# Optimization experiments

Hardware: AMD Instinct MI355X
Metric: run time of the kernel (lower is better)

The kernel has to match this reference:

```python
import jax, jax.numpy as jnp
import numpy as np

# ---- hash-grid constants (from tcnn Encoding config in __init__) ----
N_LEVELS = 16
F = 2                      # n_features_per_level
LOG2_T = 19
T = 1 << LOG2_T            # hashmap entries per level
BASE_RES = 16
PER_LEVEL_SCALE = 1.447269237440378
PRIMES = np.array([1, 2654435761, 805459861], dtype=np.uint32)
# corner offsets of the unit cube, shape [8, 3]
OFFS = np.stack(np.meshgrid([0, 1], [0, 1], [0, 1], indexing='ij'), -1).reshape(8, 3)


def hash_grid_encode(x01, table):
    """x01: [N,3] in [0,1]; table: [L, T, F]. Returns [N, L*F]."""
    offs = jnp.asarray(OFFS, dtype=jnp.int32)          # [8,3]
    primes = jnp.asarray(PRIMES)                       # [3] uint32
    feats = []
    for l in range(N_LEVELS):
        scale = BASE_RES * (PER_LEVEL_SCALE ** l) - 1.0   # tcnn grid scale
        res = int(np.ceil(scale)) + 1                      # grid resolution
        pos = x01 * scale + 0.5                            # [N,3]
        pos0 = jnp.floor(pos)
        w = pos - pos0                                     # trilinear fracs [N,3]
        pos0 = pos0.astype(jnp.int32)
        corners = jnp.clip(pos0[:, None, :] + offs[None], 0, res - 1)  # [N,8,3]
        if res ** 3 <= T:
            # dense (stride) indexing fits in the table
            idx = (corners[..., 0]
                   + res * corners[..., 1]
                   + res * res * corners[..., 2]).astype(jnp.int32)    # [N,8]
        else:
            # spatial hash with uint32 wraparound multiply + xor
            cu = corners.astype(jnp.uint32)
            idx = ((cu[..., 0] * primes[0])
                   ^ (cu[..., 1] * primes[1])
                   ^ (cu[..., 2] * primes[2])) & jnp.uint32(T - 1)
            idx = idx.astype(jnp.int32)
        # trilinear weights: prod over dims of (w if offset==1 else 1-w)
        wc = jnp.where(offs[None].astype(bool), w[:, None, :], 1.0 - w[:, None, :])
        wc = wc.prod(-1)                                   # [N,8]
        g = table[l][idx]                                  # gather -> [N,8,F]
        feats.append(jnp.einsum('nc,ncf->nf', wc, g))      # [N,F]
    return jnp.concatenate(feats, -1)                      # [N, L*F]


def mlp2(x, w1, w2):
    # 2-layer bias-free MLP with ReLU, matching MLP(num_layers=2, bias=False)
    return jnp.maximum(x @ w1, 0.0) @ w2


def setup_inputs() -> dict:
    key = jax.random.key(0)
    ks = jax.random.split(key, 6)
    N = 1048576
    points = jax.random.uniform(ks[0], (N, 3), jnp.float32, -1.0, 1.0)  # in bbox [-1,1]^3
    # tcnn hash-grid init: uniform(-1e-4, 1e-4)
    hash_table = jax.random.uniform(ks[1], (N_LEVELS, T, F), jnp.float32, -1e-4, 1e-4)
    enc_dim = N_LEVELS * F  # 32
    dw1 = jax.random.normal(ks[2], (enc_dim, 64), jnp.float32) * (1.0 / np.sqrt(enc_dim))
    dw2 = jax.random.normal(ks[3], (64, 1), jnp.float32) * (1.0 / 8.0)
    fw1 = jax.random.normal(ks[4], (enc_dim, 64), jnp.float32) * (1.0 / np.sqrt(enc_dim))
    fw2 = jax.random.normal(ks[5], (64, 3), jnp.float32) * (1.0 / 8.0)
    return {"points": points, "hash_table": hash_table,
            "dw1": dw1, "dw2": dw2, "fw1": fw1, "fw2": fw2}


def reference(points, hash_table, dw1, dw2, fw1, fw2):
    # contract_to_unisphere with bbox [[-1,-1,-1],[1,1,1]] -> [0,1]^3, clamped
    x01 = jnp.clip((points + 1.0) * 0.5, 0.0, 1.0)
    enc = hash_grid_encode(x01, hash_table)               # [N, 32]
    density = jax.nn.softplus(mlp2(enc, dw1, dw2))        # [N, 1]
    color = jax.nn.sigmoid(mlp2(enc, fw1, fw2))           # [N, 3]
    return color, density
```

## Files before the change

### kernel.cpp

```cpp
#include <hip/hip_runtime.h>
#include <hip/hip_bf16.h>
#include <cmath>

#define NLV 16
#define TBL_SIZE (1u << 19)
#define NB (1 << 18)

struct LevelConsts {
    float scale[NLV];
    int   res[NLV];
    int   dense[NLV];
};

__device__ __forceinline__ unsigned int f32_to_bf16_rne(float f) {
    unsigned int u = __float_as_uint(f);
    return (u + 0x7FFFu + ((u >> 16) & 1u)) >> 16;
}
__device__ __forceinline__ unsigned int pack_bf16(float a, float b) {
    return f32_to_bf16_rne(a) | (f32_to_bf16_rne(b) << 16);
}
__device__ __forceinline__ short f32_to_bf16_s(float f) {
    return (short)f32_to_bf16_rne(f);
}
__device__ __forceinline__ float bf16lo_to_f32(unsigned int g) {
    return __uint_as_float(g << 16);
}
__device__ __forceinline__ float bf16hi_to_f32(unsigned int g) {
    return __uint_as_float(g & 0xFFFF0000u);
}

typedef __attribute__((ext_vector_type(8))) short bf16x8;
typedef __attribute__((ext_vector_type(4))) float f32x4;
typedef __attribute__((ext_vector_type(2))) unsigned int u32x2;
typedef __attribute__((ext_vector_type(4))) unsigned int u32x4;

__global__ __launch_bounds__(256) void cvt_table(const float* __restrict__ in,
                                                 unsigned int* __restrict__ out, int npairs,
                                                 unsigned int* __restrict__ hist) {
    if (hist) {
        int h = blockIdx.x * 256 + threadIdx.x;
        if (h < NB) hist[h] = 0u;
    }
    int n2 = npairs >> 1;
    int i = blockIdx.x * 256 + threadIdx.x;
    int stride = gridDim.x * 256;
    const f32x4* in4 = (const f32x4*)in;
    u32x2* out2 = (u32x2*)out;
    for (; i < n2; i += stride) {
        f32x4 v = __builtin_nontemporal_load(&in4[i]);
        u32x2 o;
        o.x = pack_bf16(v.x, v.y);
        o.y = pack_bf16(v.z, v.w);
        __builtin_nontemporal_store(o, &out2[i]);
    }
}

__device__ __forceinline__ unsigned spread3(unsigned x) {
    x &= 0x3FFu;
    x = (x | (x << 16)) & 0x030000FFu;
    x = (x | (x << 8))  & 0x0300F00Fu;
    x = (x | (x << 4))  & 0x030C30C3u;
    x = (x | (x << 2))  & 0x09249249u;
    return x;
}
__device__ __forceinline__ unsigned bucket_key(float px, float py, float pz) {
    float x = fminf(fmaxf((px + 1.0f) * 0.5f, 0.0f), 1.0f);
    float y = fminf(fmaxf((py + 1.0f) * 0.5f, 0.0f), 1.0f);
    float z = fminf(fmaxf((pz + 1.0f) * 0.5f, 0.0f), 1.0f);
    int ix = min((int)(x * 64.0f), 63);
    int iy = min((int)(y * 64.0f), 63);
    int iz = min((int)(z * 64.0f), 63);
    return spread3((unsigned)ix) | (spread3((unsigned)iy) << 1) | (spread3((unsigned)iz) << 2);
}

__global__ __launch_bounds__(256) void bucket_hist(const float* __restrict__ pts,
                                                   unsigned* __restrict__ hist, int N) {
    int i = blockIdx.x * 256 + threadIdx.x;
    int stride = gridDim.x * 256;
    for (; i < N; i += stride) {
        float px = pts[3 * i + 0];
        float py = pts[3 * i + 1];
        float pz = pts[3 * i + 2];
        atomicAdd(&hist[bucket_key(px, py, pz)], 1u);
    }
}

__device__ __forceinline__ unsigned block_excl_scan_256(unsigned v, unsigned* wtot) {
    int t = threadIdx.x;
    int lane = t & 63, wid = t >> 6;
    unsigned x = v;
#pragma unroll
    for (int d = 1; d < 64; d <<= 1) {
        unsigned y = __shfl_up(x, d, 64);
        if (lane >= d) x += y;
    }
    unsigned wex = x - v;
    if (lane == 63) wtot[wid] = x;
    __syncthreads();
    if (t == 0) {
        unsigned r = 0;
        for (int i = 0; i < 4; i++) { unsigned tt = wtot[i]; wtot[i] = r; r += tt; }
    }
    __syncthreads();
    return wex + wtot[wid];
}

__global__ __launch_bounds__(256) void scan1(const unsigned* __restrict__ hist,
                                             unsigned* __restrict__ base,
                                             unsigned* __restrict__ bsum) {
    __shared__ unsigned wtot[4];
    int t = threadIdx.x, b = blockIdx.x;
    unsigned v = hist[b * 256 + t];
    unsigned ex = block_excl_scan_256(v, wtot);
    base[b * 256 + t] = ex;
    if (t == 255) bsum[b] = ex + v;
}

__global__ __launch_bounds__(256) void scan2(unsigned* __restrict__ bsum) {
    __shared__ unsigned wtot[4];
    int t = threadIdx.x;
    unsigned s[4];
    unsigned tot = 0;
#pragma unroll
    for (int j = 0; j < 4; j++) { s[j] = bsum[4 * t + j]; tot += s[j]; }
    unsigned ex = block_excl_scan_256(tot, wtot);
    unsigned run = ex;
#pragma unroll
    for (int j = 0; j < 4; j++) { unsigned sv = s[j]; bsum[4 * t + j] = run; run += sv; }
}

__global__ __launch_bounds__(256) void scan3(unsigned* __restrict__ base,
                                             const unsigned* __restrict__ bsum) {
    base[blockIdx.x * 256 + threadIdx.x] += bsum[blockIdx.x];
}

__global__ __launch_bounds__(256) void bucket_scatter(const float* __restrict__ pts,
                                                      unsigned* __restrict__ base,
                                                      f32x4* __restrict__ spts4, int N) {
    int i = blockIdx.x * 256 + threadIdx.x;
    int stride = gridDim.x * 256;
    for (; i < N; i += stride) {
        float px = pts[3 * i + 0];
        float py = pts[3 * i + 1];
        float pz = pts[3 * i + 2];
        unsigned k = bucket_key(px, py, pz);
        unsigned pos = atomicAdd(&base[k], 1u);
        f32x4 o;
        o.x = px; o.y = py; o.z = pz; o.w = __uint_as_float((unsigned)i);
        spts4[pos] = o;
    }
}

#define ENC_P 4
template<int PSTRIDE>
__global__ __launch_bounds__(256) void encode_lvl(
    const float* __restrict__ points,
    const unsigned int* __restrict__ tbl,
    unsigned int* __restrict__ enc,
    int N, LevelConsts C)
{
    const int level = blockIdx.y;
    const float sc    = C.scale[level];
    const int   res   = C.res[level];
    const int   dense = C.dense[level];
    const unsigned int* __restrict__ t = tbl + (size_t)level * TBL_SIZE;
    unsigned int* __restrict__ eo = enc + (size_t)level * N;

    const int base = blockIdx.x * (256 * ENC_P) + threadIdx.x;

    int   pt[ENC_P];
    int   valid[ENC_P];
    float wx[ENC_P], wy[ENC_P], wz[ENC_P];
    unsigned int i0a[ENC_P][4], i1a[ENC_P][4];

#pragma unroll
    for (int q = 0; q < ENC_P; q++) {
        pt[q] = base + q * 256;
        valid[q] = pt[q] < N;
        int p = valid[q] ? pt[q] : 0;
        float px, py, pz;
        if (PSTRIDE == 4) {
            f32x4 v = *(const f32x4*)&points[(size_t)p * 4];
            px = v.x; py = v.y; pz = v.z;
        } else {
            px = points[p * 3 + 0];
            py = points[p * 3 + 1];
            pz = points[p * 3 + 2];
        }
        float x = fminf(fmaxf((px + 1.0f) * 0.5f, 0.0f), 1.0f);
        float y = fminf(fmaxf((py + 1.0f) * 0.5f, 0.0f), 1.0f);
        float z = fminf(fmaxf((pz + 1.0f) * 0.5f, 0.0f), 1.0f);

        float fx = x * sc + 0.5f;
        float fy = y * sc + 0.5f;
        float fz = z * sc + 0.5f;
        float f0x = floorf(fx), f0y = floorf(fy), f0z = floorf(fz);
        wx[q] = fx - f0x; wy[q] = fy - f0y; wz[q] = fz - f0z;
        int ix0 = min(max((int)f0x, 0), res - 1);
        int iy0 = min(max((int)f0y, 0), res - 1);
        int iz0 = min(max((int)f0z, 0), res - 1);
        int ix1 = min(ix0 + 1, res - 1);
        int iy1 = min(iy0 + 1, res - 1);
        int iz1 = min(iz0 + 1, res - 1);

#pragma unroll
        for (int m = 0; m < 4; m++) {
            unsigned int uy = (unsigned int)((m & 1) ? iy1 : iy0);
            unsigned int uz = (unsigned int)((m & 2) ? iz1 : iz0);
            unsigned int i0, i1;
            if (dense) {
                unsigned int b = (unsigned int)res * uy + (unsigned int)(res * res) * uz;
                i0 = (unsigned int)ix0 + b;
                i1 = (unsigned int)ix1 + b;
            } else {
                unsigned int H = uy * 2654435761u ^ uz * 805459861u;
                i0 = ((unsigned int)ix0 ^ H) & (TBL_SIZE - 1u);
                i1 = ((unsigned int)ix1 ^ H) & (TBL_SIZE - 1u);
            }
            i0a[q][m] = i0;
            i1a[q][m] = i1;
        }
    }

    u32x2 pr[ENC_P][4];
#pragma unroll
    for (int q = 0; q < ENC_P; q++)
#pragma unroll
        for (int m = 0; m < 4; m++)
            pr[q][m] = *(const u32x2*)(t + (i0a[q][m] & ~1u));

    unsigned int ex[ENC_P][4];
#pragma unroll
    for (int q = 0; q < ENC_P; q++)
#pragma unroll
        for (int m = 0; m < 4; m++) {
            unsigned int i0 = i0a[q][m], i1 = i1a[q][m];
            unsigned int e = 0u;
            if (i1 != (i0 ^ 1u)) e = t[i1];
            ex[q][m] = e;
        }

#pragma unroll
    for (int q = 0; q < ENC_P; q++) {
        float e0 = 0.0f, e1 = 0.0f;
        float wxq = wx[q];
#pragma unroll
        for (int m = 0; m < 4; m++) {
            unsigned int i0 = i0a[q][m], i1 = i1a[q][m];
            u32x2 P = pr[q][m];
            unsigned int v0   = (i0 & 1u) ? P.y : P.x;
            unsigned int vpar = (i0 & 1u) ? P.x : P.y;
            unsigned int v1   = (i1 == (i0 ^ 1u)) ? vpar : ex[q][m];
            float wyz = (((m & 1) ? wy[q] : 1.0f - wy[q])) *
                        (((m & 2) ? wz[q] : 1.0f - wz[q]));
            float w0 = wyz * (1.0f - wxq);
            float w1 = wyz * wxq;
            e0 = fmaf(w0, bf16lo_to_f32(v0), e0);
            e0 = fmaf(w1, bf16lo_to_f32(v1), e0);
            e1 = fmaf(w0, bf16hi_to_f32(v0), e1);
            e1 = fmaf(w1, bf16hi_to_f32(v1), e1);
        }
        if (valid[q]) __builtin_nontemporal_store(pack_bf16(e0, e1), &eo[pt[q]]);
    }
}

__global__ __launch_bounds__(256, 4) void mlp_kernel(
    const unsigned int* __restrict__ enc,
    const float* __restrict__ dw1, const float* __restrict__ dw2,
    const float* __restrict__ fw1, const float* __restrict__ fw2,
    const unsigned int* __restrict__ perm,
    float* __restrict__ out, int N, int ntiles)
{
    __shared__ unsigned int hsh[4][16][68];
    __shared__ float sOut[4][256];

    const int tid  = threadIdx.x;
    const int wave = tid >> 6;
    const int lane = tid & 63;
    const int l15 = lane & 15;
    const int quad = lane >> 4;

    bf16x8 B1[8];
#pragma unroll
    for (int nt = 0; nt < 8; nt++) {
        int col = nt * 16 + l15;
        const float* w = (col < 64) ? (dw1 + col) : (fw1 + (col - 64));
#pragma unroll
        for (int j = 0; j < 8; j++) {
            int k = quad * 8 + j;
            B1[nt][j] = f32_to_bf16_s(w[k * 64]);
        }
    }

    bf16x8 B2[4];
#pragma unroll
    for (int s = 0; s < 4; s++) {
#pragma unroll
        for (int j = 0; j < 8; j++) {
            int k_lds = s * 32 + quad * 8 + j;
            int hu = ((k_lds & 7) << 4) | (k_lds >> 3);
            float v = 0.0f;
            if (l15 == 0)      v = (hu < 64)  ? dw2[hu] : 0.0f;
            else if (l15 < 4)  v = (hu >= 64) ? fw2[(hu - 64) * 3 + (l15 - 1)] : 0.0f;
            B2[s][j] = f32_to_bf16_s(v);
        }
    }

    for (int tile = blockIdx.x; tile < ntiles; tile += gridDim.x) {
        const int wbase = tile * 256 + wave * 64;

        unsigned int au[4][4];
#pragma unroll
        for (int sub = 0; sub < 4; sub++) {
            int ptc = min(wbase + sub * 16 + l15, N - 1);
#pragma unroll
            for (int j = 0; j < 4; j++)
                au[sub][j] = enc[(size_t)(quad * 4 + j) * N + ptc];
        }

#pragma unroll
        for (int sub = 0; sub < 4; sub++) {
            union { unsigned int u[4]; bf16x8 v; } acvt;
#pragma unroll
            for (int j = 0; j < 4; j++) acvt.u[j] = au[sub][j];

            f32x4 acc1[8];
#pragma unroll
            for (int nt = 0; nt < 8; nt++) {
                acc1[nt] = (f32x4){0.0f, 0.0f, 0.0f, 0.0f};
                acc1[nt] = __builtin_amdgcn_mfma_f32_16x16x32_bf16(acvt.v, B1[nt], acc1[nt], 0, 0, 0);
            }

#pragma unroll
            for (int r = 0; r < 4; r++) {
                u32x4 pk;
#pragma unroll
                for (int d = 0; d < 4; d++) {
                    float h0 = fmaxf(acc1[2 * d + 0][r], 0.0f);
                    float h1 = fmaxf(acc1[2 * d + 1][r], 0.0f);
                    pk[d] = pack_bf16(h0, h1);
                }
                *(u32x4*)&hsh[wave][quad * 4 + r][l15 * 4] = pk;
            }

            f32x4 p0 = (f32x4){0,0,0,0}, p1 = (f32x4){0,0,0,0};
            f32x4 p2 = (f32x4){0,0,0,0}, p3 = (f32x4){0,0,0,0};
            {
                bf16x8 a0 = *(const bf16x8*)&hsh[wave][l15][0 * 16 + quad * 4];
                bf16x8 a1 = *(const bf16x8*)&hsh[wave][l15][1 * 16 + quad * 4];
                bf16x8 a2 = *(const bf16x8*)&hsh[wave][l15][2 * 16 + quad * 4];
                bf16x8 a3 = *(const bf16x8*)&hsh[wave][l15][3 * 16 + quad * 4];
                p0 = __builtin_amdgcn_mfma_f32_16x16x32_bf16(a0, B2[0], p0, 0, 0, 0);
                p1 = __builtin_amdgcn_mfma_f32_16x16x32_bf16(a1, B2[1], p1, 0, 0, 0);
                p2 = __builtin_amdgcn_mfma_f32_16x16x32_bf16(a2, B2[2], p2, 0, 0, 0);
                p3 = __builtin_amdgcn_mfma_f32_16x16x32_bf16(a3, B2[3], p3, 0, 0, 0);
            }
            f32x4 acc2;
#pragma unroll
            for (int r = 0; r < 4; r++) acc2[r] = (p0[r] + p1[r]) + (p2[r] + p3[r]);

            if (l15 < 4) {
#pragma unroll
                for (int r = 0; r < 4; r++)
                    sOut[wave][(sub * 16 + quad * 4 + r) * 4 + l15] = acc2[r];
            }
        }

        if (perm) {
            int p = wbase + lane;
            if (p < N) {
                unsigned int o = perm[(size_t)p * 4 + 3];
                f32x4 v = *(const f32x4*)&sOut[wave][lane * 4];
                float d = v[0];
                d = (d > 20.0f) ? d : log1pf(expf(d));
                out[(size_t)3 * N + o] = d;
                float r0 = 1.0f / (1.0f + expf(-v[1]));
                float g0 = 1.0f / (1.0f + expf(-v[2]));
                float b0 = 1.0f / (1.0f + expf(-v[3]));
                out[(size_t)o * 3 + 0] = r0;
                out[(size_t)o * 3 + 1] = g0;
                out[(size_t)o * 3 + 2] = b0;
            }
        } else {
            long long cmax = ((long long)N - wbase) * 3;
#pragma unroll
            for (int round = 0; round < 3; round++) {
                int f = round * 64 + lane;
                int lp = f / 3, c = f - lp * 3;
                float v = sOut[wave][lp * 4 + 1 + c];
                v = 1.0f / (1.0f + expf(-v));
                if (f < cmax) out[(size_t)wbase * 3 + f] = v;
            }
            {
                int p = wbase + lane;
                float v = sOut[wave][lane * 4];
                v = (v > 20.0f) ? v : log1pf(expf(v));
                if (p < N) out[(size_t)3 * N + p] = v;
            }
        }
    }
}

__global__ __launch_bounds__(256) void nerf_fused(
    const float* __restrict__ points,
    const float* __restrict__ table,
    const float* __restrict__ dw1, const float* __restrict__ dw2,
    const float* __restrict__ fw1, const float* __restrict__ fw2,
    float* __restrict__ out, int N, LevelConsts C)
{
    __shared__ float sD[64 * 32];
    __shared__ float sF[64 * 32];
    __shared__ float sDw2[64];
    __shared__ float sFw2[64 * 3];

    for (int idx = threadIdx.x; idx < 2048; idx += 256) {
        int i = idx >> 6;
        int j = idx & 63;
        sD[j * 32 + i] = dw1[idx];
        sF[j * 32 + i] = fw1[idx];
    }
    if (threadIdx.x < 64)  sDw2[threadIdx.x] = dw2[threadIdx.x];
    if (threadIdx.x < 192) sFw2[threadIdx.x] = fw2[threadIdx.x];
    __syncthreads();

    int gid = blockIdx.x * 256 + threadIdx.x;
    if (gid >= N) return;

    float px = points[gid * 3 + 0];
    float py = points[gid * 3 + 1];
    float pz = points[gid * 3 + 2];
    float x = fminf(fmaxf((px + 1.0f) * 0.5f, 0.0f), 1.0f);
    float y = fminf(fmaxf((py + 1.0f) * 0.5f, 0.0f), 1.0f);
    float z = fminf(fmaxf((pz + 1.0f) * 0.5f, 0.0f), 1.0f);

    float enc[32];

#pragma unroll
    for (int l = 0; l < NLV; l++) {
        const float sc = C.scale[l];
        const int   res = C.res[l];
        const int   dense = C.dense[l];
        const float* __restrict__ tbl = table + (size_t)l * TBL_SIZE * 2;

        float fx = x * sc + 0.5f;
        float fy = y * sc + 0.5f;
        float fz = z * sc + 0.5f;
        float f0x = floorf(fx), f0y = floorf(fy), f0z = floorf(fz);
        float wx = fx - f0x, wy = fy - f0y, wz = fz - f0z;
        int ix0 = min(max((int)f0x, 0), res - 1);
        int iy0 = min(max((int)f0y, 0), res - 1);
        int iz0 = min(max((int)f0z, 0), res - 1);
        int ix1 = min(ix0 + 1, res - 1);
        int iy1 = min(iy0 + 1, res - 1);
        int iz1 = min(iz0 + 1, res - 1);

        float e0 = 0.0f, e1 = 0.0f;
#pragma unroll
        for (int c = 0; c < 8; c++) {
            int cx = (c & 4) ? ix1 : ix0;
            int cy = (c & 2) ? iy1 : iy0;
            int cz = (c & 1) ? iz1 : iz0;
            float wgt = (((c & 4) ? wx : 1.0f - wx) *
                         ((c & 2) ? wy : 1.0f - wy)) *
                         ((c & 1) ? wz : 1.0f - wz);
            unsigned int idx;
            if (dense) {
                idx = (unsigned int)(cx + res * cy + res * res * cz);
            } else {
                idx = ((unsigned int)cx * 1u
                     ^ (unsigned int)cy * 2654435761u
                     ^ (unsigned int)cz * 805459861u) & (TBL_SIZE - 1u);
            }
            const float2 g = *(const float2*)(tbl + (size_t)idx * 2);
            e0 = fmaf(wgt, g.x, e0);
            e1 = fmaf(wgt, g.y, e1);
        }
        enc[2 * l + 0] = e0;
        enc[2 * l + 1] = e1;
    }

    float dacc = 0.0f, c0 = 0.0f, c1 = 0.0f, c2 = 0.0f;
    for (int j = 0; j < 64; j++) {
        float hd = 0.0f, hf = 0.0f;
        const float* __restrict__ colD = &sD[j * 32];
        const float* __restrict__ colF = &sF[j * 32];
#pragma unroll
        for (int i = 0; i < 32; i++) {
            hd = fmaf(enc[i], colD[i], hd);
            hf = fmaf(enc[i], colF[i], hf);
        }
        hd = fmaxf(hd, 0.0f);
        hf = fmaxf(hf, 0.0f);
        dacc = fmaf(hd, sDw2[j], dacc);
        c0 = fmaf(hf, sFw2[j * 3 + 0], c0);
        c1 = fmaf(hf, sFw2[j * 3 + 1], c1);
        c2 = fmaf(hf, sFw2[j * 3 + 2], c2);
    }

    float density = (dacc > 20.0f) ? dacc : log1pf(expf(dacc));
    out[gid * 3 + 0] = 1.0f / (1.0f + expf(-c0));
    out[gid * 3 + 1] = 1.0f / (1.0f + expf(-c1));
    out[gid * 3 + 2] = 1.0f / (1.0f + expf(-c2));
    out[(size_t)3 * N + gid] = density;
}

extern "C" void kernel_launch(void* const* d_in, const int* in_sizes, int n_in,
                              void* d_out, int out_size, void* d_ws, size_t ws_size,
                              hipStream_t stream) {
    const float* points = (const float*)d_in[0];
    const float* table  = (const float*)d_in[1];
    const float* dw1    = (const float*)d_in[2];
    const float* dw2    = (const float*)d_in[3];
    const float* fw1    = (const float*)d_in[4];
    const float* fw2    = (const float*)d_in[5];
    int N = in_sizes[0] / 3;

    LevelConsts C;
    for (int l = 0; l < NLV; l++) {
        double s = 16.0 * pow(1.447269237440378, (double)l) - 1.0;
        C.scale[l] = (float)s;
        int res = (int)ceil(s) + 1;
        C.res[l] = res;
        C.dense[l] = ((long long)res * res * res <= (long long)TBL_SIZE) ? 1 : 0;
    }

    auto align256 = [](size_t x) { return (x + 255) & ~(size_t)255; };
    const size_t tbl_bytes  = align256((size_t)NLV * TBL_SIZE * 4);
    const size_t enc_bytes  = align256((size_t)N * NLV * 4);
    const size_t spts_bytes = align256((size_t)N * 4 * 4);
    const size_t hist_bytes = align256((size_t)NB * 4);
    const size_t base_bytes = align256((size_t)NB * 4);
    const size_t bsum_bytes = align256((size_t)(NB / 256) * 4);
    const size_t sort_total = tbl_bytes + enc_bytes + spts_bytes
                            + hist_bytes + base_bytes + bsum_bytes;

    if (ws_size >= sort_total) {
        char* wp = (char*)d_ws;
        unsigned int* tbl_bf16 = (unsigned int*)wp;            wp += tbl_bytes;
        unsigned int* enc_ws   = (unsigned int*)wp;            wp += enc_bytes;
        f32x4*        spts4    = (f32x4*)wp;                   wp += spts_bytes;
        unsigned int* hist     = (unsigned int*)wp;            wp += hist_bytes;
        unsigned int* base     = (unsigned int*)wp;            wp += base_bytes;
        unsigned int* bsum     = (unsigned int*)wp;            wp += bsum_bytes;

        int npairs = NLV * TBL_SIZE;
        cvt_table<<<1024, 256, 0, stream>>>(table, tbl_bf16, npairs, hist);

        int pblocks = min((N + 255) / 256, 2048);
        bucket_hist<<<pblocks, 256, 0, stream>>>(points, hist, N);
        scan1<<<NB / 256, 256, 0, stream>>>(hist, base, bsum);
        scan2<<<1, 256, 0, stream>>>(bsum);
        scan3<<<NB / 256, 256, 0, stream>>>(base, bsum);
        bucket_scatter<<<pblocks, 256, 0, stream>>>(points, base, spts4, N);

        int chunks = (N + 256 * ENC_P - 1) / (256 * ENC_P);
        encode_lvl<4><<<dim3(chunks, NLV), 256, 0, stream>>>((const float*)spts4,
                                                             tbl_bf16, enc_ws, N, C);

        int ntiles = (N + 255) / 256;
        mlp_kernel<<<1792, 256, 0, stream>>>(enc_ws, dw1, dw2, fw1, fw2,
                                             (const unsigned int*)spts4,
                                             (float*)d_out, N, ntiles);
    } else if (ws_size >= tbl_bytes + enc_bytes) {
        unsigned int* tbl_bf16 = (unsigned int*)d_ws;
        unsigned int* enc_ws   = (unsigned int*)((char*)d_ws + tbl_bytes);

        int npairs = NLV * TBL_SIZE;
        cvt_table<<<1024, 256, 0, stream>>>(table, tbl_bf16, npairs, nullptr);

        int chunks = (N + 256 * ENC_P - 1) / (256 * ENC_P);
        encode_lvl<3><<<dim3(chunks, NLV), 256, 0, stream>>>(points, tbl_bf16, enc_ws, N, C);

        int ntiles = (N + 255) / 256;
        mlp_kernel<<<1792, 256, 0, stream>>>(enc_ws, dw1, dw2, fw1, fw2, nullptr,
                                             (float*)d_out, N, ntiles);
    } else {
        int blocks = (N + 255) / 256;
        nerf_fused<<<blocks, 256, 0, stream>>>(points, table, dw1, dw2, fw1, fw2,
                                               (float*)d_out, N, C);
    }
}
```

Before: 567.7 us.

## Fuse hash-grid encoding with MLP in one kernel over spatially sorted points

Replaces the separate per-level encode kernel and MLP kernel on the sorted path with one kernel. Each block encodes 256 sorted points across all 16 levels, in groups of four, into LDS and then runs the MFMA MLP directly. This removes the global round trip of the encoded features (N*16 words written and reread) and one launch. The cost is that one block now walks all levels' tables, so there is less table locality per level than with per-level grids, and the larger LDS footprint plus register pressure caps occupancy at 3 blocks.

```diff
diff --git a/kernel.cpp b/kernel.cpp
--- a/kernel.cpp
+++ b/kernel.cpp
@@ -151,8 +151,207 @@
     }
 }
 
+__global__ __launch_bounds__(256, 3) void fused_enc_mlp(
+    const f32x4* __restrict__ spts4,
+    const unsigned int* __restrict__ tbl,
+    const float* __restrict__ dw1, const float* __restrict__ dw2,
+    const float* __restrict__ fw1, const float* __restrict__ fw2,
+    float* __restrict__ out, int N, int ntiles, LevelConsts C)
+{
+    __shared__ unsigned int encLds[NLV][258];
+    __shared__ unsigned int hsh[4][16][68];
+    __shared__ float sOut[4][256];
+
+    const int tid  = threadIdx.x;
+    const int wave = tid >> 6;
+    const int lane = tid & 63;
+    const int l15 = lane & 15;
+    const int quad = lane >> 4;
+
+    bf16x8 B1[8];
+#pragma unroll
+    for (int nt = 0; nt < 8; nt++) {
+        int col = nt * 16 + l15;
+        const float* w = (col < 64) ? (dw1 + col) : (fw1 + (col - 64));
+#pragma unroll
+        for (int j = 0; j < 8; j++) {
+            int k = quad * 8 + j;
+            B1[nt][j] = f32_to_bf16_s(w[k * 64]);
+        }
+    }
+
+    bf16x8 B2[4];
+#pragma unroll
+    for (int s = 0; s < 4; s++) {
+#pragma unroll
+        for (int j = 0; j < 8; j++) {
+            int k_lds = s * 32 + quad * 8 + j;
+            int hu = ((k_lds & 7) << 4) | (k_lds >> 3);
+            float v = 0.0f;
+            if (l15 == 0)      v = (hu < 64)  ? dw2[hu] : 0.0f;
+            else if (l15 < 4)  v = (hu >= 64) ? fw2[(hu - 64) * 3 + (l15 - 1)] : 0.0f;
+            B2[s][j] = f32_to_bf16_s(v);
+        }
+    }
+
+    for (int tile = blockIdx.x; tile < ntiles; tile += gridDim.x) {
+        const int p  = tile * 256 + tid;
+        const int pc = min(p, N - 1);
+        f32x4 pv = __builtin_nontemporal_load(&spts4[pc]);
+        const float x = fminf(fmaxf((pv.x + 1.0f) * 0.5f, 0.0f), 1.0f);
+        const float y = fminf(fmaxf((pv.y + 1.0f) * 0.5f, 0.0f), 1.0f);
+        const float z = fminf(fmaxf((pv.z + 1.0f) * 0.5f, 0.0f), 1.0f);
+
+        for (int lg = 0; lg < 4; lg++) {
+            float wxa[4], wya[4], wza[4];
+            unsigned int i0a[4][4], i1a[4][4];
+#pragma unroll
+            for (int lv = 0; lv < 4; lv++) {
+                int l = lg * 4 + lv;
+                float sc  = C.scale[l];
+                int  res  = C.res[l];
+                int  dense = C.dense[l];
+                float fx = x * sc + 0.5f;
+                float fy = y * sc + 0.5f;
+                float fz = z * sc + 0.5f;
+                float f0x = floorf(fx), f0y = floorf(fy), f0z = floorf(fz);
+                wxa[lv] = fx - f0x; wya[lv] = fy - f0y; wza[lv] = fz - f0z;
+                int ix0 = min(max((int)f0x, 0), res - 1);
+                int iy0 = min(max((int)f0y, 0), res - 1);
+                int iz0 = min(max((int)f0z, 0), res - 1);
+                int ix1 = min(ix0 + 1, res - 1);
+                int iy1 = min(iy0 + 1, res - 1);
+                int iz1 = min(iz0 + 1, res - 1);
+#pragma unroll
+                for (int m = 0; m < 4; m++) {
+                    unsigned int uy = (unsigned int)((m & 1) ? iy1 : iy0);
+                    unsigned int uz = (unsigned int)((m & 2) ? iz1 : iz0);
+                    unsigned int i0, i1;
+                    if (dense) {
+                        unsigned int b = (unsigned int)res * uy + (unsigned int)(res * res) * uz;
+                        i0 = (unsigned int)ix0 + b;
+                        i1 = (unsigned int)ix1 + b;
+                    } else {
+                        unsigned int H = uy * 2654435761u ^ uz * 805459861u;
+                        i0 = ((unsigned int)ix0 ^ H) & (TBL_SIZE - 1u);
+                        i1 = ((unsigned int)ix1 ^ H) & (TBL_SIZE - 1u);
+                    }
+                    i0a[lv][m] = i0;
+                    i1a[lv][m] = i1;
+                }
+            }
+
+            u32x2 pr[4][4];
+#pragma unroll
+            for (int lv = 0; lv < 4; lv++) {
+                const unsigned int* tl = tbl + (size_t)(lg * 4 + lv) * TBL_SIZE;
+#pragma unroll
+                for (int m = 0; m < 4; m++)
+                    pr[lv][m] = *(const u32x2*)(tl + (i0a[lv][m] & ~1u));
+            }
+            unsigned int ex[4][4];
+#pragma unroll
+            for (int lv = 0; lv < 4; lv++) {
+                const unsigned int* tl = tbl + (size_t)(lg * 4 + lv) * TBL_SIZE;
+#pragma unroll
+                for (int m = 0; m < 4; m++) {
+                    unsigned int i0 = i0a[lv][m], i1 = i1a[lv][m];
+                    unsigned int e = 0u;
+                    if (i1 != (i0 ^ 1u)) e = tl[i1];
+                    ex[lv][m] = e;
+                }
+            }
+
+#pragma unroll
+            for (int lv = 0; lv < 4; lv++) {
+                float e0 = 0.0f, e1 = 0.0f;
+                float wxq = wxa[lv];
+#pragma unroll
+                for (int m = 0; m < 4; m++) {
+                    unsigned int i0 = i0a[lv][m], i1 = i1a[lv][m];
+                    u32x2 P = pr[lv][m];
+                    unsigned int v0   = (i0 & 1u) ? P.y : P.x;
+                    unsigned int vpar = (i0 & 1u) ? P.x : P.y;
+                    unsigned int v1   = (i1 == (i0 ^ 1u)) ? vpar : ex[lv][m];
+                    float wyz = (((m & 1) ? wya[lv] : 1.0f - wya[lv])) *
+                                (((m & 2) ? wza[lv] : 1.0f - wza[lv]));
+                    float w0 = wyz * (1.0f - wxq);
+                    float w1 = wyz * wxq;
+                    e0 = fmaf(w0, bf16lo_to_f32(v0), e0);
+                    e0 = fmaf(w1, bf16lo_to_f32(v1), e0);
+                    e1 = fmaf(w0, bf16hi_to_f32(v0), e1);
+                    e1 = fmaf(w1, bf16hi_to_f32(v1), e1);
+                }
+                encLds[lg * 4 + lv][tid] = pack_bf16(e0, e1);
+            }
+        }
+
+#pragma unroll
+        for (int sub = 0; sub < 4; sub++) {
+            union { unsigned int u[4]; bf16x8 v; } acvt;
+#pragma unroll
+            for (int j = 0; j < 4; j++)
+                acvt.u[j] = encLds[quad * 4 + j][wave * 64 + sub * 16 + l15];
+
+            f32x4 acc1[8];
+#pragma unroll
+            for (int nt = 0; nt < 8; nt++) {
+                acc1[nt] = (f32x4){0.0f, 0.0f, 0.0f, 0.0f};
+                acc1[nt] = __builtin_amdgcn_mfma_f32_16x16x32_bf16(acvt.v, B1[nt], acc1[nt], 0, 0, 0);
+            }
+
+#pragma unroll
+            for (int r = 0; r < 4; r++) {
+                u32x4 pk;
+#pragma unroll
+                for (int d = 0; d < 4; d++) {
+                    float h0 = fmaxf(acc1[2 * d + 0][r], 0.0f);
+                    float h1 = fmaxf(acc1[2 * d + 1][r], 0.0f);
+                    pk[d] = pack_bf16(h0, h1);
+                }
+                *(u32x4*)&hsh[wave][quad * 4 + r][l15 * 4] = pk;
+            }
+
+            f32x4 p0 = (f32x4){0,0,0,0}, p1 = (f32x4){0,0,0,0};
+            f32x4 p2 = (f32x4){0,0,0,0}, p3 = (f32x4){0,0,0,0};
+            {
+                bf16x8 a0 = *(const bf16x8*)&hsh[wave][l15][0 * 16 + quad * 4];
+                bf16x8 a1 = *(const bf16x8*)&hsh[wave][l15][1 * 16 + quad * 4];
+                bf16x8 a2 = *(const bf16x8*)&hsh[wave][l15][2 * 16 + quad * 4];
+                bf16x8 a3 = *(const bf16x8*)&hsh[wave][l15][3 * 16 + quad * 4];
+                p0 = __builtin_amdgcn_mfma_f32_16x16x32_bf16(a0, B2[0], p0, 0, 0, 0);
+                p1 = __builtin_amdgcn_mfma_f32_16x16x32_bf16(a1, B2[1], p1, 0, 0, 0);
+                p2 = __builtin_amdgcn_mfma_f32_16x16x32_bf16(a2, B2[2], p2, 0, 0, 0);
+                p3 = __builtin_amdgcn_mfma_f32_16x16x32_bf16(a3, B2[3], p3, 0, 0, 0);
+            }
+            f32x4 acc2;
+#pragma unroll
+            for (int r = 0; r < 4; r++) acc2[r] = (p0[r] + p1[r]) + (p2[r] + p3[r]);
+
+            if (l15 < 4) {
+#pragma unroll
+                for (int r = 0; r < 4; r++)
+                    sOut[wave][(sub * 16 + quad * 4 + r) * 4 + l15] = acc2[r];
+            }
+        }
+
+        if (p < N) {
+            unsigned int o = __float_as_uint(pv.w);
+            f32x4 v = *(const f32x4*)&sOut[wave][lane * 4];
+            float d = v[0];
+            d = (d > 20.0f) ? d : log1pf(expf(d));
+            out[(size_t)3 * N + o] = d;
+            float r0 = 1.0f / (1.0f + expf(-v[1]));
+            float g0 = 1.0f / (1.0f + expf(-v[2]));
+            float b0 = 1.0f / (1.0f + expf(-v[3]));
+            out[(size_t)o * 3 + 0] = r0;
+            out[(size_t)o * 3 + 1] = g0;
+            out[(size_t)o * 3 + 2] = b0;
+        }
+    }
+}
+
 #define ENC_P 4
-template<int PSTRIDE>
 __global__ __launch_bounds__(256) void encode_lvl(
     const float* __restrict__ points,
     const unsigned int* __restrict__ tbl,
@@ -178,15 +377,9 @@
         pt[q] = base + q * 256;
         valid[q] = pt[q] < N;
         int p = valid[q] ? pt[q] : 0;
-        float px, py, pz;
-        if (PSTRIDE == 4) {
-            f32x4 v = *(const f32x4*)&points[(size_t)p * 4];
-            px = v.x; py = v.y; pz = v.z;
-        } else {
-            px = points[p * 3 + 0];
-            py = points[p * 3 + 1];
-            pz = points[p * 3 + 2];
-        }
+        float px = points[p * 3 + 0];
+        float py = points[p * 3 + 1];
+        float pz = points[p * 3 + 2];
         float x = fminf(fmaxf((px + 1.0f) * 0.5f, 0.0f), 1.0f);
         float y = fminf(fmaxf((py + 1.0f) * 0.5f, 0.0f), 1.0f);
         float z = fminf(fmaxf((pz + 1.0f) * 0.5f, 0.0f), 1.0f);
@@ -268,7 +461,6 @@
     const unsigned int* __restrict__ enc,
     const float* __restrict__ dw1, const float* __restrict__ dw2,
     const float* __restrict__ fw1, const float* __restrict__ fw2,
-    const unsigned int* __restrict__ perm,
     float* __restrict__ out, int N, int ntiles)
 {
     __shared__ unsigned int hsh[4][16][68];
@@ -366,37 +558,20 @@
             }
         }
 
-        if (perm) {
+        long long cmax = ((long long)N - wbase) * 3;
+#pragma unroll
+        for (int round = 0; round < 3; round++) {
+            int f = round * 64 + lane;
+            int lp = f / 3, c = f - lp * 3;
+            float v = sOut[wave][lp * 4 + 1 + c];
+            v = 1.0f / (1.0f + expf(-v));
+            if (f < cmax) out[(size_t)wbase * 3 + f] = v;
+        }
+        {
             int p = wbase + lane;
-            if (p < N) {
-                unsigned int o = perm[(size_t)p * 4 + 3];
-                f32x4 v = *(const f32x4*)&sOut[wave][lane * 4];
-                float d = v[0];
-                d = (d > 20.0f) ? d : log1pf(expf(d));
-                out[(size_t)3 * N + o] = d;
-                float r0 = 1.0f / (1.0f + expf(-v[1]));
-                float g0 = 1.0f / (1.0f + expf(-v[2]));
-                float b0 = 1.0f / (1.0f + expf(-v[3]));
-                out[(size_t)o * 3 + 0] = r0;
-                out[(size_t)o * 3 + 1] = g0;
-                out[(size_t)o * 3 + 2] = b0;
-            }
-        } else {
-            long long cmax = ((long long)N - wbase) * 3;
-#pragma unroll
-            for (int round = 0; round < 3; round++) {
-                int f = round * 64 + lane;
-                int lp = f / 3, c = f - lp * 3;
-                float v = sOut[wave][lp * 4 + 1 + c];
-                v = 1.0f / (1.0f + expf(-v));
-                if (f < cmax) out[(size_t)wbase * 3 + f] = v;
-            }
-            {
-                int p = wbase + lane;
-                float v = sOut[wave][lane * 4];
-                v = (v > 20.0f) ? v : log1pf(expf(v));
-                if (p < N) out[(size_t)3 * N + p] = v;
-            }
+            float v = sOut[wave][lane * 4];
+            v = (v > 20.0f) ? v : log1pf(expf(v));
+            if (p < N) out[(size_t)3 * N + p] = v;
         }
     }
 }
@@ -526,18 +701,18 @@
 
     auto align256 = [](size_t x) { return (x + 255) & ~(size_t)255; };
     const size_t tbl_bytes  = align256((size_t)NLV * TBL_SIZE * 4);
-    const size_t enc_bytes  = align256((size_t)N * NLV * 4);
     const size_t spts_bytes = align256((size_t)N * 4 * 4);
     const size_t hist_bytes = align256((size_t)NB * 4);
     const size_t base_bytes = align256((size_t)NB * 4);
     const size_t bsum_bytes = align256((size_t)(NB / 256) * 4);
-    const size_t sort_total = tbl_bytes + enc_bytes + spts_bytes
-                            + hist_bytes + base_bytes + bsum_bytes;
+    const size_t enc_bytes  = align256((size_t)N * NLV * 4);
+    const size_t sort_total = tbl_bytes + spts_bytes + hist_bytes + base_bytes + bsum_bytes;
+
+    int ntiles = (N + 255) / 256;
 
     if (ws_size >= sort_total) {
         char* wp = (char*)d_ws;
         unsigned int* tbl_bf16 = (unsigned int*)wp;            wp += tbl_bytes;
-        unsigned int* enc_ws   = (unsigned int*)wp;            wp += enc_bytes;
         f32x4*        spts4    = (f32x4*)wp;                   wp += spts_bytes;
         unsigned int* hist     = (unsigned int*)wp;            wp += hist_bytes;
         unsigned int* base     = (unsigned int*)wp;            wp += base_bytes;
@@ -553,14 +728,9 @@
         scan3<<<NB / 256, 256, 0, stream>>>(base, bsum);
         bucket_scatter<<<pblocks, 256, 0, stream>>>(points, base, spts4, N);
 
-        int chunks = (N + 256 * ENC_P - 1) / (256 * ENC_P);
-        encode_lvl<4><<<dim3(chunks, NLV), 256, 0, stream>>>((const float*)spts4,
-                                                             tbl_bf16, enc_ws, N, C);
-
-        int ntiles = (N + 255) / 256;
-        mlp_kernel<<<1792, 256, 0, stream>>>(enc_ws, dw1, dw2, fw1, fw2,
-                                             (const unsigned int*)spts4,
-                                             (float*)d_out, N, ntiles);
+        int fblocks = min(ntiles, 2048);
+        fused_enc_mlp<<<fblocks, 256, 0, stream>>>(spts4, tbl_bf16, dw1, dw2, fw1, fw2,
+                                                   (float*)d_out, N, ntiles, C);
     } else if (ws_size >= tbl_bytes + enc_bytes) {
         unsigned int* tbl_bf16 = (unsigned int*)d_ws;
         unsigned int* enc_ws   = (unsigned int*)((char*)d_ws + tbl_bytes);
@@ -569,10 +739,9 @@
         cvt_table<<<1024, 256, 0, stream>>>(table, tbl_bf16, npairs, nullptr);
 
         int chunks = (N + 256 * ENC_P - 1) / (256 * ENC_P);
-        encode_lvl<3><<<dim3(chunks, NLV), 256, 0, stream>>>(points, tbl_bf16, enc_ws, N, C);
-
-        int ntiles = (N + 255) / 256;
-        mlp_kernel<<<1792, 256, 0, stream>>>(enc_ws, dw1, dw2, fw1, fw2, nullptr,
+        encode_lvl<<<dim3(chunks, NLV), 256, 0, stream>>>(points, tbl_bf16, enc_ws, N, C);
+
+        mlp_kernel<<<1792, 256, 0, stream>>>(enc_ws, dw1, dw2, fw1, fw2,
                                              (float*)d_out, N, ntiles);
     } else {
         int blocks = (N + 255) / 256;
```

New measurement: 808.6 us. 1.42x slower.

## Replace global bucket sort with per-block local sort fused with table conversion

Applied to the files above, without the earlier changes.

Replaces the global 2^18-bucket counting sort (histogram, three-pass scan, scatter) with a per-block shared-memory counting sort over 8192-point chunks on a coarser 4096-key Morton grid. That sort runs in the same launch as the bf16 table conversion, cutting five launches and the global atomics. The encode kernel now uses a flat grid and maps block IDs so each XCD handles a pair of levels, aiming to keep each level's table slice in one XCD's L2. The trade-off is that locality becomes per-chunk rather than global, which may raise gather misses in encode.

```diff
diff --git a/kernel.cpp b/kernel.cpp
--- a/kernel.cpp
+++ b/kernel.cpp
@@ -4,7 +4,10 @@
 
 #define NLV 16
 #define TBL_SIZE (1u << 19)
-#define NB (1 << 18)
+
+#define SORT_PPB 8192
+#define SORT_THREADS 512
+#define SORT_NKEYS 4096
 
 struct LevelConsts {
     float scale[NLV];
@@ -34,13 +37,113 @@
 typedef __attribute__((ext_vector_type(2))) unsigned int u32x2;
 typedef __attribute__((ext_vector_type(4))) unsigned int u32x4;
 
+__device__ __forceinline__ unsigned spread3(unsigned x) {
+    x &= 0x3FFu;
+    x = (x | (x << 16)) & 0x030000FFu;
+    x = (x | (x << 8))  & 0x0300F00Fu;
+    x = (x | (x << 4))  & 0x030C30C3u;
+    x = (x | (x << 2))  & 0x09249249u;
+    return x;
+}
+__device__ __forceinline__ unsigned key12(float px, float py, float pz) {
+    float x = fminf(fmaxf((px + 1.0f) * 0.5f, 0.0f), 1.0f);
+    float y = fminf(fmaxf((py + 1.0f) * 0.5f, 0.0f), 1.0f);
+    float z = fminf(fmaxf((pz + 1.0f) * 0.5f, 0.0f), 1.0f);
+    int ix = min((int)(x * 16.0f), 15);
+    int iy = min((int)(y * 16.0f), 15);
+    int iz = min((int)(z * 16.0f), 15);
+    return spread3((unsigned)ix) | (spread3((unsigned)iy) << 1) | (spread3((unsigned)iz) << 2);
+}
+
+__global__ __launch_bounds__(SORT_THREADS) void cvt_and_sort(
+    const float* __restrict__ tablef32, unsigned int* __restrict__ tbl_out, int npairs,
+    const float* __restrict__ pts, f32x4* __restrict__ spts4, int N, int sortBlocks)
+{
+    __shared__ unsigned hist[SORT_NKEYS];
+    __shared__ unsigned wsum[SORT_THREADS / 64];
+
+    if ((int)blockIdx.x < sortBlocks) {
+        const int sb   = blockIdx.x;
+        const int base = sb * SORT_PPB;
+        const int cnt  = min(SORT_PPB, N - base);
+        const int tid  = threadIdx.x;
+        const int lane = tid & 63, wid = tid >> 6;
+
+        for (int i = tid; i < SORT_NKEYS; i += SORT_THREADS) hist[i] = 0u;
+        __syncthreads();
+
+        unsigned short keys[16];
+#pragma unroll
+        for (int q = 0; q < 16; q++) {
+            int idx = q * SORT_THREADS + tid;
+            unsigned k = 0xFFFFu;
+            if (idx < cnt) {
+                int p = base + idx;
+                float px = pts[3 * p + 0];
+                float py = pts[3 * p + 1];
+                float pz = pts[3 * p + 2];
+                k = key12(px, py, pz);
+                atomicAdd(&hist[k], 1u);
+            }
+            keys[q] = (unsigned short)k;
+        }
+        __syncthreads();
+
+        unsigned loc[8], s = 0;
+#pragma unroll
+        for (int j = 0; j < 8; j++) { loc[j] = hist[tid * 8 + j]; s += loc[j]; }
+        unsigned x = s;
+#pragma unroll
+        for (int d = 1; d < 64; d <<= 1) {
+            unsigned y = __shfl_up(x, d, 64);
+            if (lane >= d) x += y;
+        }
+        unsigned wex = x - s;
+        if (lane == 63) wsum[wid] = x;
+        __syncthreads();
+        if (tid == 0) {
+            unsigned r = 0;
+            for (int i = 0; i < SORT_THREADS / 64; i++) { unsigned t = wsum[i]; wsum[i] = r; r += t; }
+        }
+        __syncthreads();
+        unsigned run = wex + wsum[wid];
+#pragma unroll
+        for (int j = 0; j < 8; j++) { hist[tid * 8 + j] = run; run += loc[j]; }
+        __syncthreads();
+
+#pragma unroll
+        for (int q = 0; q < 16; q++) {
+            int idx = q * SORT_THREADS + tid;
+            if (idx < cnt) {
+                int p = base + idx;
+                float px = pts[3 * p + 0];
+                float py = pts[3 * p + 1];
+                float pz = pts[3 * p + 2];
+                unsigned pos = atomicAdd(&hist[keys[q]], 1u);
+                f32x4 o;
+                o.x = px; o.y = py; o.z = pz; o.w = __uint_as_float((unsigned)p);
+                spts4[base + pos] = o;
+            }
+        }
+    } else {
+        int b = blockIdx.x - sortBlocks;
+        int n2 = npairs >> 1;
+        int i = b * SORT_THREADS + threadIdx.x;
+        int stride = ((int)gridDim.x - sortBlocks) * SORT_THREADS;
+        const f32x4* in4 = (const f32x4*)tablef32;
+        u32x2* out2 = (u32x2*)tbl_out;
+        for (; i < n2; i += stride) {
+            f32x4 v = __builtin_nontemporal_load(&in4[i]);
+            u32x2 o;
+            o.x = pack_bf16(v.x, v.y);
+            o.y = pack_bf16(v.z, v.w);
+            __builtin_nontemporal_store(o, &out2[i]);
+        }
+    }
+}
+
 __global__ __launch_bounds__(256) void cvt_table(const float* __restrict__ in,
-                                                 unsigned int* __restrict__ out, int npairs,
-                                                 unsigned int* __restrict__ hist) {
-    if (hist) {
-        int h = blockIdx.x * 256 + threadIdx.x;
-        if (h < NB) hist[h] = 0u;
-    }
+                                                 unsigned int* __restrict__ out, int npairs) {
     int n2 = npairs >> 1;
     int i = blockIdx.x * 256 + threadIdx.x;
     int stride = gridDim.x * 256;
@@ -55,102 +158,6 @@
     }
 }
 
-__device__ __forceinline__ unsigned spread3(unsigned x) {
-    x &= 0x3FFu;
-    x = (x | (x << 16)) & 0x030000FFu;
-    x = (x | (x << 8))  & 0x0300F00Fu;
-    x = (x | (x << 4))  & 0x030C30C3u;
-    x = (x | (x << 2))  & 0x09249249u;
-    return x;
-}
-__device__ __forceinline__ unsigned bucket_key(float px, float py, float pz) {
-    float x = fminf(fmaxf((px + 1.0f) * 0.5f, 0.0f), 1.0f);
-    float y = fminf(fmaxf((py + 1.0f) * 0.5f, 0.0f), 1.0f);
-    float z = fminf(fmaxf((pz + 1.0f) * 0.5f, 0.0f), 1.0f);
-    int ix = min((int)(x * 64.0f), 63);
-    int iy = min((int)(y * 64.0f), 63);
-    int iz = min((int)(z * 64.0f), 63);
-    return spread3((unsigned)ix) | (spread3((unsigned)iy) << 1) | (spread3((unsigned)iz) << 2);
-}
-
-__global__ __launch_bounds__(256) void bucket_hist(const float* __restrict__ pts,
-                                                   unsigned* __restrict__ hist, int N) {
-    int i = blockIdx.x * 256 + threadIdx.x;
-    int stride = gridDim.x * 256;
-    for (; i < N; i += stride) {
-        float px = pts[3 * i + 0];
-        float py = pts[3 * i + 1];
-        float pz = pts[3 * i + 2];
-        atomicAdd(&hist[bucket_key(px, py, pz)], 1u);
-    }
-}
-
-__device__ __forceinline__ unsigned block_excl_scan_256(unsigned v, unsigned* wtot) {
-    int t = threadIdx.x;
-    int lane = t & 63, wid = t >> 6;
-    unsigned x = v;
-#pragma unroll
-    for (int d = 1; d < 64; d <<= 1) {
-        unsigned y = __shfl_up(x, d, 64);
-        if (lane >= d) x += y;
-    }
-    unsigned wex = x - v;
-    if (lane == 63) wtot[wid] = x;
-    __syncthreads();
-    if (t == 0) {
-        unsigned r = 0;
-        for (int i = 0; i < 4; i++) { unsigned tt = wtot[i]; wtot[i] = r; r += tt; }
-    }
-    __syncthreads();
-    return wex + wtot[wid];
-}
-
-__global__ __launch_bounds__(256) void scan1(const unsigned* __restrict__ hist,
-                                             unsigned* __restrict__ base,
-                                             unsigned* __restrict__ bsum) {
-    __shared__ unsigned wtot[4];
-    int t = threadIdx.x, b = blockIdx.x;
-    unsigned v = hist[b * 256 + t];
-    unsigned ex = block_excl_scan_256(v, wtot);
-    base[b * 256 + t] = ex;
-    if (t == 255) bsum[b] = ex + v;
-}
-
-__global__ __launch_bounds__(256) void scan2(unsigned* __restrict__ bsum) {
-    __shared__ unsigned wtot[4];
-    int t = threadIdx.x;
-    unsigned s[4];
-    unsigned tot = 0;
-#pragma unroll
-    for (int j = 0; j < 4; j++) { s[j] = bsum[4 * t + j]; tot += s[j]; }
-    unsigned ex = block_excl_scan_256(tot, wtot);
-    unsigned run = ex;
-#pragma unroll
-    for (int j = 0; j < 4; j++) { unsigned sv = s[j]; bsum[4 * t + j] = run; run += sv; }
-}
-
-__global__ __launch_bounds__(256) void scan3(unsigned* __restrict__ base,
-                                             const unsigned* __restrict__ bsum) {
-    base[blockIdx.x * 256 + threadIdx.x] += bsum[blockIdx.x];
-}
-
-__global__ __launch_bounds__(256) void bucket_scatter(const float* __restrict__ pts,
-                                                      unsigned* __restrict__ base,
-                                                      f32x4* __restrict__ spts4, int N) {
-    int i = blockIdx.x * 256 + threadIdx.x;
-    int stride = gridDim.x * 256;
-    for (; i < N; i += stride) {
-        float px = pts[3 * i + 0];
-        float py = pts[3 * i + 1];
-        float pz = pts[3 * i + 2];
-        unsigned k = bucket_key(px, py, pz);
-        unsigned pos = atomicAdd(&base[k], 1u);
-        f32x4 o;
-        o.x = px; o.y = py; o.z = pz; o.w = __uint_as_float((unsigned)i);
-        spts4[pos] = o;
-    }
-}
-
 #define ENC_P 4
 template<int PSTRIDE>
 __global__ __launch_bounds__(256) void encode_lvl(
@@ -159,14 +166,19 @@
     unsigned int* __restrict__ enc,
     int N, LevelConsts C)
 {
-    const int level = blockIdx.y;
+    const int bid  = blockIdx.x;
+    const int xcd  = bid & 7;
+    const int half = (bid >> 3) & 1;
+    const int level = half ? (15 - xcd) : xcd;
+    const int chunk = bid >> 4;
+
     const float sc    = C.scale[level];
     const int   res   = C.res[level];
     const int   dense = C.dense[level];
     const unsigned int* __restrict__ t = tbl + (size_t)level * TBL_SIZE;
     unsigned int* __restrict__ eo = enc + (size_t)level * N;
 
-    const int base = blockIdx.x * (256 * ENC_P) + threadIdx.x;
+    const int base = chunk * (256 * ENC_P) + threadIdx.x;
 
     int   pt[ENC_P];
     int   valid[ENC_P];
@@ -528,36 +540,24 @@
     const size_t tbl_bytes  = align256((size_t)NLV * TBL_SIZE * 4);
     const size_t enc_bytes  = align256((size_t)N * NLV * 4);
     const size_t spts_bytes = align256((size_t)N * 4 * 4);
-    const size_t hist_bytes = align256((size_t)NB * 4);
-    const size_t base_bytes = align256((size_t)NB * 4);
-    const size_t bsum_bytes = align256((size_t)(NB / 256) * 4);
-    const size_t sort_total = tbl_bytes + enc_bytes + spts_bytes
-                            + hist_bytes + base_bytes + bsum_bytes;
-
-    if (ws_size >= sort_total) {
+
+    int ntiles = (N + 255) / 256;
+    int chunks = (N + 256 * ENC_P - 1) / (256 * ENC_P);
+    int npairs = NLV * TBL_SIZE;
+
+    if (ws_size >= tbl_bytes + enc_bytes + spts_bytes) {
         char* wp = (char*)d_ws;
         unsigned int* tbl_bf16 = (unsigned int*)wp;            wp += tbl_bytes;
         unsigned int* enc_ws   = (unsigned int*)wp;            wp += enc_bytes;
         f32x4*        spts4    = (f32x4*)wp;                   wp += spts_bytes;
-        unsigned int* hist     = (unsigned int*)wp;            wp += hist_bytes;
-        unsigned int* base     = (unsigned int*)wp;            wp += base_bytes;
-        unsigned int* bsum     = (unsigned int*)wp;            wp += bsum_bytes;
-
-        int npairs = NLV * TBL_SIZE;
-        cvt_table<<<1024, 256, 0, stream>>>(table, tbl_bf16, npairs, hist);
-
-        int pblocks = min((N + 255) / 256, 2048);
-        bucket_hist<<<pblocks, 256, 0, stream>>>(points, hist, N);
-        scan1<<<NB / 256, 256, 0, stream>>>(hist, base, bsum);
-        scan2<<<1, 256, 0, stream>>>(bsum);
-        scan3<<<NB / 256, 256, 0, stream>>>(base, bsum);
-        bucket_scatter<<<pblocks, 256, 0, stream>>>(points, base, spts4, N);
-
-        int chunks = (N + 256 * ENC_P - 1) / (256 * ENC_P);
-        encode_lvl<4><<<dim3(chunks, NLV), 256, 0, stream>>>((const float*)spts4,
-                                                             tbl_bf16, enc_ws, N, C);
-
-        int ntiles = (N + 255) / 256;
+
+        int sortBlocks = (N + SORT_PPB - 1) / SORT_PPB;
+        cvt_and_sort<<<sortBlocks + 1024, SORT_THREADS, 0, stream>>>(
+            table, tbl_bf16, npairs, points, spts4, N, sortBlocks);
+
+        encode_lvl<4><<<chunks * NLV, 256, 0, stream>>>((const float*)spts4,
+                                                        tbl_bf16, enc_ws, N, C);
+
         mlp_kernel<<<1792, 256, 0, stream>>>(enc_ws, dw1, dw2, fw1, fw2,
                                              (const unsigned int*)spts4,
                                              (float*)d_out, N, ntiles);
@@ -565,13 +565,10 @@
         unsigned int* tbl_bf16 = (unsigned int*)d_ws;
         unsigned int* enc_ws   = (unsigned int*)((char*)d_ws + tbl_bytes);
 
-        int npairs = NLV * TBL_SIZE;
-        cvt_table<<<1024, 256, 0, stream>>>(table, tbl_bf16, npairs, nullptr);
-
-        int chunks = (N + 256 * ENC_P - 1) / (256 * ENC_P);
-        encode_lvl<3><<<dim3(chunks, NLV), 256, 0, stream>>>(points, tbl_bf16, enc_ws, N, C);
-
-        int ntiles = (N + 255) / 256;
+        cvt_table<<<1024, 256, 0, stream>>>(table, tbl_bf16, npairs);
+
+        encode_lvl<3><<<chunks * NLV, 256, 0, stream>>>(points, tbl_bf16, enc_ws, N, C);
+
         mlp_kernel<<<1792, 256, 0, stream>>>(enc_ws, dw1, dw2, fw1, fw2, nullptr,
                                              (float*)d_out, N, ntiles);
     } else {
```

After: 633.1 us. 11.5% more time.
